# Kernel tuning notes

Measured on AMD Instinct MI355X. Metric: run time of the kernel, lower is better.

## Reference

```python
import jax, jax.numpy as jnp
import numpy as np
from jax import lax

# static dims (match init_kwargs)
B, F, C, H, W = 10, 64, 3, 180, 180   # batch=10 (hard-coded by reshape), arr_size frames
CH, OUT, NCLS = 64, 256, 5            # channel, out_size, len(ansmap)+1
K1, K2, POOL = 9, 5, 2                # second*diff, third, pool
EPS = 1e-5


def setup_inputs() -> dict:
    key = jax.random.key(0)
    ks = jax.random.split(key, 12)
    s = lambda k, shape: jax.random.normal(k, shape, dtype=jnp.float32) * 0.05
    return {
        "x": jax.random.normal(ks[0], (B, F, C, H, W), dtype=jnp.float32),
        "W1": s(ks[1], (CH, C, K1, K1)),
        "b1": s(ks[2], (CH,)),
        "W2": s(ks[3], (3, CH, K2, K2)),
        "b2": s(ks[4], (3,)),
        "gamma": jnp.ones((F,), jnp.float32),
        "beta": jnp.zeros((F,), jnp.float32),
        "Wih": s(ks[5], (3, OUT, 1)),
        "Whh": s(ks[6], (3, OUT, OUT)),
        "bih": s(ks[7], (3, OUT)),
        "bhh": s(ks[8], (3, OUT)),
        "Wl": s(ks[9], (NCLS, OUT)),
        "bl": s(ks[10], (NCLS,)),
    }


def _maxpool2(y):
    return lax.reduce_window(y, -jnp.inf, lax.max, (1, 1, POOL, POOL), (1, 1, POOL, POOL), 'VALID')


def reference(x, W1, b1, W2, b2, gamma, beta, Wih, Whh, bih, bhh, Wl, bl):
    # conv stack applied per frame; batch all B*F frames at once
    xc = x.reshape(B * F, C, H, W)
    y = lax.conv_general_dilated(xc, W1, (K1, K1), 'VALID') + b1[None, :, None, None]
    y = _maxpool2(jax.nn.relu(y))                      # [B*F, CH, 10, 10]
    y = lax.conv_general_dilated(y, W2, (K2, K2), 'VALID') + b2[None, :, None, None]
    y = _maxpool2(jax.nn.relu(y))                      # [B*F, 3, 1, 1]
    y = y.reshape(B, F, 3)

    # BatchNorm1d(arr_size) in train mode: normalize each of the F channels over (batch, length)
    mean = y.mean(axis=(0, 2), keepdims=True)
    var = y.var(axis=(0, 2), keepdims=True)
    y = (y - mean) / jnp.sqrt(var + EPS) * gamma[None, :, None] + beta[None, :, None]

    # per-sample reorder of the 3 channels by (max - min) range over time
    t = y.transpose(0, 2, 1)                           # [B, 3, F]
    rng = t.max(-1) - t.min(-1)                        # [B, 3]
    perm = jnp.argsort(rng, axis=1)                    # [B, 3]
    ts = jnp.take_along_axis(t, perm[:, :, None], axis=1)  # [B, 3, F]

    # rank r goes through RNN r; vmap the scan over the 3 RNNs
    seqs = ts.transpose(1, 2, 0)[..., None]            # [3, F, B, 1]

    def rnn_last(seq, wih, whh, bi, bh):               # seq: [F, B, 1]
        def step(h, xt):
            return jnp.tanh(xt @ wih.T + bi + h @ whh.T + bh), None
        h, _ = lax.scan(step, jnp.zeros((B, OUT), seq.dtype), seq)
        return h                                       # last hidden == output at t=-1

    lasts = jax.vmap(rnn_last)(seqs, Wih, Whh, bih, bhh)  # [3, B, OUT]
    avg = lasts.mean(axis=0)                           # AvgPool2d((3,1)) + Flatten -> [B, OUT]
    return avg @ Wl.T + bl                             # [B, NCLS]
```

## Files before the change

### kernel.cpp

```cpp
#include <hip/hip_runtime.h>

typedef __attribute__((ext_vector_type(8))) short bf16x8;
typedef __attribute__((ext_vector_type(4))) float f32x4;

#define MFMA16(a,b,c) __builtin_amdgcn_mfma_f32_16x16x32_bf16((a),(b),(c),0,0,0)

__device__ __forceinline__ unsigned short f2bf(float f){
  unsigned int u = __float_as_uint(f);
  unsigned int r = (u + 0x7fffu + ((u>>16)&1u)) >> 16;
  return (unsigned short)r;
}
__device__ __forceinline__ float bf2f(unsigned short h){
  return __uint_as_float(((unsigned int)h)<<16);
}
__device__ __forceinline__ float tanh_fast(float x){
  float e = __expf(2.f*x);
  return 1.f - 2.f/(e + 1.f);
}

#define WS_W1H   0u
#define WS_W1L   32768u
#define WS_WHHH  65536u
#define WS_WHHL  458752u
#define WS_Y1    851968u
#define WS_Y2    17235968u
#define WS_SEQ   17243648u
#define WS_LAST  17255936u

__global__ __launch_bounds__(256) void k_prep(const float* __restrict__ W1,
                                              const float* __restrict__ Whh,
                                              unsigned short* __restrict__ w1h,
                                              unsigned short* __restrict__ w1l,
                                              unsigned short* __restrict__ whh_h,
                                              unsigned short* __restrict__ whh_l){
  int t = blockIdx.x*256 + threadIdx.x;
  if (t < 2048){
    int l = t & 63, kt = (t>>6)&7, mt = t>>9;
    int co = mt*16 + (l&15);
    int k0 = kt*32 + ((l>>4)<<3);
    bf16x8 hv, lv;
    #pragma unroll
    for (int j=0;j<8;j++){
      int k = k0 + j;
      float v = (k < 243) ? W1[co*243 + k] : 0.f;
      unsigned short h = f2bf(v);
      unsigned short lo = f2bf(v - bf2f(h));
      hv[j] = (short)h; lv[j] = (short)lo;
    }
    *(bf16x8*)(w1h + (size_t)t*8) = hv;
    *(bf16x8*)(w1l + (size_t)t*8) = lv;
  } else if (t < 2048 + 24576){
    int u = t - 2048;
    int l = u & 63, kt = (u>>6)&7, nt = (u>>9)&15, rnn = u>>13;
    int o = nt*16 + (l&15);
    int k0 = kt*32 + ((l>>4)<<3);
    const float* src = Whh + ((size_t)rnn*256 + o)*256;
    bf16x8 hv, lv;
    #pragma unroll
    for (int j=0;j<8;j++){
      float v = src[k0 + j];
      unsigned short h = f2bf(v);
      unsigned short lo = f2bf(v - bf2f(h));
      hv[j] = (short)h; lv[j] = (short)lo;
    }
    *(bf16x8*)(whh_h + (size_t)u*8) = hv;
    *(bf16x8*)(whh_l + (size_t)u*8) = lv;
  }
}

__global__ __launch_bounds__(256,4) void k_conv1(const float* __restrict__ x,
                                                 const float* __restrict__ b1,
                                                 const unsigned short* __restrict__ w1h,
                                                 const unsigned short* __restrict__ w1l,
                                                 float* __restrict__ y1){
  __shared__ __align__(16) char smem[40960];
  int fr = blockIdx.x / 10, g = blockIdx.x % 10;
  int t = threadIdx.x, w = t>>6, l = t&63;

  bf16x8 ah[8], al[8];
  #pragma unroll
  for (int kt=0; kt<8; kt++){
    size_t fi = (((size_t)(w*8 + kt))*64 + l)*8;
    ah[kt] = *(const bf16x8*)(w1h + fi);
    al[kt] = *(const bf16x8*)(w1l + fi);
  }
  float bias[4];
  #pragma unroll
  for (int reg=0;reg<4;reg++) bias[reg] = b1[w*16 + ((l>>4)<<2) + reg];

  const float4* xb4 = (const float4*)x + (size_t)fr*24300 + (size_t)g*810;
  for (int i=t; i<2430; i+=256){
    int c = i/810;
    int rem = i - c*810;
    int rl = rem/45;
    int quad = rem - rl*45;
    int oyl = (rl >= 9) ? 1 : 0;
    int ky = rl - 9*oyl;
    float4 v4 = xb4[c*8100 + rem];
    int kbase = c*81 + ky*9;
    int col0 = quad<<2;
    int ox = (col0*57)>>9;
    int kx = col0 - 9*ox;
    int p = oyl*20 + ox;
    float vv[4] = {v4.x, v4.y, v4.z, v4.w};
    #pragma unroll
    for (int q=0;q<4;q++){
      int k = kbase + kx;
      int off = ((p<<9) + (k<<1)) ^ ((p&7)<<4);
      unsigned int u = __float_as_uint(vv[q]);
      *(unsigned short*)(smem + off) = (unsigned short)(u>>16);
      float lof = vv[q] - __uint_as_float(u & 0xffff0000u);
      *(unsigned short*)(smem + 20480 + off) = (unsigned short)(__float_as_uint(lof)>>16);
      kx++; if (kx==9){ kx=0; p++; }
    }
  }
  for (int i=t; i<520; i+=256){
    int p = i/13, k = 243 + (i - p*13);
    int off = ((p<<9) + (k<<1)) ^ ((p&7)<<4);
    *(unsigned short*)(smem + off) = 0;
    *(unsigned short*)(smem + 20480 + off) = 0;
  }
  __syncthreads();

  const int pbase[3] = {0, 16, 24};
  int colb = (l>>4)<<4;
  f32x4 acc[3];
  #pragma unroll
  for (int nt=0;nt<3;nt++) acc[nt] = (f32x4){0.f,0.f,0.f,0.f};
  #pragma unroll
  for (int nt=0; nt<3; nt++){
    int p = pbase[nt] + (l&15);
    int sw = (p&7)<<4;
    #pragma unroll
    for (int kt=0; kt<8; kt++){
      int off = ((p<<9) + (kt<<6) + colb) ^ sw;
      bf16x8 bh  = *(const bf16x8*)(smem + off);
      bf16x8 blo = *(const bf16x8*)(smem + 20480 + off);
      acc[nt] = MFMA16(ah[kt], bh,  acc[nt]);
      acc[nt] = MFMA16(ah[kt], blo, acc[nt]);
      acc[nt] = MFMA16(al[kt], bh,  acc[nt]);
    }
  }
  __syncthreads();

  float* poolb = (float*)smem;
  #pragma unroll
  for (int nt=0;nt<3;nt++){
    int m = l&15;
    int p = pbase[nt] + m;
    #pragma unroll
    for (int reg=0;reg<4;reg++){
      int co = w*16 + ((l>>4)<<2) + reg;
      float v = fmaxf(acc[nt][reg] + bias[reg], 0.f);
      if (nt != 2 || m >= 8) poolb[co*41 + p] = v;
    }
  }
  __syncthreads();
  for (int idx=t; idx<640; idx+=256){
    int co = idx/10, xp = idx - co*10;
    const float* pb = poolb + co*41;
    float m = fmaxf(fmaxf(pb[2*xp], pb[2*xp+1]), fmaxf(pb[20+2*xp], pb[21+2*xp]));
    y1[(size_t)fr*6400 + co*100 + g*10 + xp] = m;
  }
}

__global__ __launch_bounds__(256) void k_conv2(const float* __restrict__ y1,
                                               const float* __restrict__ W2,
                                               const float* __restrict__ b2,
                                               float* __restrict__ y2){
  __shared__ float yl[6400];
  __shared__ float w2s[4800];
  int fr = blockIdx.x, t = threadIdx.x;
  const float4* src = (const float4*)(y1 + (size_t)fr*6400);
  for (int i=t;i<1600;i+=256) ((float4*)yl)[i] = src[i];
  for (int i=t;i<1200;i+=256) ((float4*)w2s)[i] = ((const float4*)W2)[i];
  __syncthreads();
  if (t < 192){
    int o = t>>4, l16 = t&15;
    int ch = o>>2, pos = o&3;
    int oy = pos>>1, ox = pos&1;
    float s = 0.f;
    for (int i=0;i<100;i++){
      int k = l16 + (i<<4);
      int ci = k/25; int r = k - ci*25; int ky = r/5, kx = r - ky*5;
      s += yl[ci*100 + (5*oy+ky)*10 + 5*ox + kx] * w2s[ch*1600 + k];
    }
    #pragma unroll
    for (int d=1; d<16; d<<=1) s += __shfl_xor(s, d);
    float v = fmaxf(s + b2[ch], 0.f);
    v = fmaxf(v, __shfl_xor(v, 16));
    v = fmaxf(v, __shfl_xor(v, 32));
    if ((t&63)==0) y2[fr*3 + (t>>6)] = v;
  }
}

__global__ __launch_bounds__(256) void k_bn(const float* __restrict__ y2,
                                            const float* __restrict__ gamma,
                                            const float* __restrict__ beta,
                                            float* __restrict__ seq){
  __shared__ float yl[1920];
  __shared__ float af[64], bfv[64];
  __shared__ float tsb[10][3][64];
  __shared__ float rngL[10][3];
  __shared__ int   perm[10][3];
  int t = threadIdx.x;
  for (int i=t;i<1920;i+=256) yl[i] = y2[i];
  __syncthreads();
  if (t < 64){
    float mu = 0.f;
    for (int b=0;b<10;b++)
      for (int ch=0;ch<3;ch++) mu += yl[(b*64 + t)*3 + ch];
    mu *= (1.f/30.f);
    float v = 0.f;
    for (int b=0;b<10;b++)
      for (int ch=0;ch<3;ch++){ float d = yl[(b*64+t)*3+ch] - mu; v += d*d; }
    v *= (1.f/30.f);
    float rs = rsqrtf(v + 1e-5f);
    float a = gamma[t]*rs;
    af[t] = a; bfv[t] = beta[t] - mu*a;
  }
  __syncthreads();
  if (t < 30){
    int b = t/3, ch = t - b*3;
    float mx = -1e30f, mn = 1e30f;
    for (int f=0; f<64; f++){
      float v = yl[(b*64+f)*3+ch]*af[f] + bfv[f];
      tsb[b][ch][f] = v;
      mx = fmaxf(mx, v); mn = fminf(mn, v);
    }
    rngL[b][ch] = mx - mn;
  }
  __syncthreads();
  if (t < 10){
    #pragma unroll
    for (int ch=0; ch<3; ch++){
      float rc = rngL[t][ch];
      int rank = 0;
      #pragma unroll
      for (int c2=0; c2<3; c2++){
        float r2 = rngL[t][c2];
        if (r2 < rc || (r2 == rc && c2 < ch)) rank++;
      }
      perm[t][rank] = ch;
    }
  }
  __syncthreads();
  for (int idx=t; idx<3072; idx+=256){
    int r = idx>>10, rem = idx & 1023, f = rem>>4, b = rem & 15;
    float v = 0.f;
    if (b < 10) v = tsb[b][perm[b][r]][f];
    seq[idx] = v;
  }
}

__global__ __launch_bounds__(512) void k_rnn(const unsigned short* __restrict__ whh_h,
                                             const unsigned short* __restrict__ whh_l,
                                             const float* __restrict__ seq,
                                             const float* __restrict__ Wih,
                                             const float* __restrict__ bih,
                                             const float* __restrict__ bhh,
                                             float* __restrict__ lasts){
  __shared__ __align__(16) char hsm[36864];
  float* seqL = (float*)(hsm + 32768);
  int rnn = blockIdx.x;
  int t = threadIdx.x, w = t>>6, l = t&63;
  bf16x8 Bh[2][8], Bl[2][8];
  #pragma unroll
  for (int q=0;q<2;q++){
    int nt = 2*w + q;
    #pragma unroll
    for (int kt=0;kt<8;kt++){
      size_t fi = (((((size_t)rnn*16 + nt)*8) + kt)*64 + l)*8;
      Bh[q][kt] = *(const bf16x8*)(whh_h + fi);
      Bl[q][kt] = *(const bf16x8*)(whh_l + fi);
    }
  }
  int o0 = (2*w)*16 + (l&15), o1 = o0 + 16;
  float wih0 = Wih[rnn*256 + o0], wih1 = Wih[rnn*256 + o1];
  float bs0 = bih[rnn*256+o0] + bhh[rnn*256+o0];
  float bs1 = bih[rnn*256+o1] + bhh[rnn*256+o1];
  for (int i=t; i<1024; i+=512) seqL[i] = seq[rnn*1024 + i];
  float4 z4 = {0.f,0.f,0.f,0.f};
  for (int i=t; i<1024; i+=512) ((float4*)hsm)[i] = z4;
  __syncthreads();
  int arow = l&15, colb = (l>>4)<<4, sw = (arow&7)<<4;
  int b_base = (l>>4)<<2;
  for (int step=0; step<64; step++){
    char* cur = hsm + ((step&1)<<14);
    char* nxt = hsm + (((step+1)&1)<<14);
    f32x4 p0=(f32x4){0,0,0,0}, q0=p0, r0=p0, p1=p0, q1=p0, r1=p0;
    #pragma unroll
    for (int kt=0; kt<8; kt++){
      int off = ((arow<<9) + (kt<<6) + colb) ^ sw;
      bf16x8 ahv = *(const bf16x8*)(cur + off);
      bf16x8 alv = *(const bf16x8*)(cur + 8192 + off);
      p0 = MFMA16(ahv, Bh[0][kt], p0);
      q0 = MFMA16(ahv, Bl[0][kt], q0);
      r0 = MFMA16(alv, Bh[0][kt], r0);
      p1 = MFMA16(ahv, Bh[1][kt], p1);
      q1 = MFMA16(ahv, Bl[1][kt], q1);
      r1 = MFMA16(alv, Bh[1][kt], r1);
    }
    float4 sx = *(const float4*)(seqL + (step<<4) + b_base);
    float sxa[4] = {sx.x, sx.y, sx.z, sx.w};
    #pragma unroll
    for (int reg=0; reg<4; reg++){
      int b = b_base + reg;
      float a0 = (p0[reg] + q0[reg]) + r0[reg];
      float a1 = (p1[reg] + q1[reg]) + r1[reg];
      float h0 = tanh_fast(a0 + sxa[reg]*wih0 + bs0);
      float h1 = tanh_fast(a1 + sxa[reg]*wih1 + bs1);
      int wsw = (b&7)<<4;
      int off0 = ((b<<9) + (o0<<1)) ^ wsw;
      int off1 = ((b<<9) + (o1<<1)) ^ wsw;
      unsigned int u0 = __float_as_uint(h0);
      unsigned int u1 = __float_as_uint(h1);
      *(unsigned short*)(nxt + off0) = (unsigned short)(u0>>16);
      float l0 = h0 - __uint_as_float(u0 & 0xffff0000u);
      *(unsigned short*)(nxt + 8192 + off0) = (unsigned short)(__float_as_uint(l0)>>16);
      *(unsigned short*)(nxt + off1) = (unsigned short)(u1>>16);
      float l1 = h1 - __uint_as_float(u1 & 0xffff0000u);
      *(unsigned short*)(nxt + 8192 + off1) = (unsigned short)(__float_as_uint(l1)>>16);
      if (step == 63){
        lasts[((size_t)rnn*16 + b)*256 + o0] = h0;
        lasts[((size_t)rnn*16 + b)*256 + o1] = h1;
      }
    }
    __syncthreads();
  }
}

__global__ __launch_bounds__(512) void k_head(const float* __restrict__ lasts,
                                              const float* __restrict__ Wl,
                                              const float* __restrict__ bl,
                                              float* __restrict__ out){
  int t = threadIdx.x;
  if (t < 400){
    int oidx = t>>3, l8 = t&7;
    int b = oidx/5, c = oidx - b*5;
    float s = 0.f;
    for (int i=0;i<32;i++){
      int o = (l8<<5) + i;
      float avg = (lasts[(size_t)(0*16+b)*256+o] + lasts[(size_t)(1*16+b)*256+o]
                 + lasts[(size_t)(2*16+b)*256+o]) * (1.f/3.f);
      s += avg * Wl[c*256 + o];
    }
    #pragma unroll
    for (int d=1; d<8; d<<=1) s += __shfl_xor(s, d);
    if (l8 == 0) out[oidx] = s + bl[c];
  }
}

extern "C" void kernel_launch(void* const* d_in, const int* in_sizes, int n_in,
                              void* d_out, int out_size, void* d_ws, size_t ws_size,
                              hipStream_t stream){
  const float* x    = (const float*)d_in[0];
  const float* W1   = (const float*)d_in[1];
  const float* b1   = (const float*)d_in[2];
  const float* W2   = (const float*)d_in[3];
  const float* b2   = (const float*)d_in[4];
  const float* gamma= (const float*)d_in[5];
  const float* beta = (const float*)d_in[6];
  const float* Wih  = (const float*)d_in[7];
  const float* Whh  = (const float*)d_in[8];
  const float* bih  = (const float*)d_in[9];
  const float* bhh  = (const float*)d_in[10];
  const float* Wl   = (const float*)d_in[11];
  const float* bl   = (const float*)d_in[12];
  char* ws = (char*)d_ws;
  unsigned short* w1h  = (unsigned short*)(ws + WS_W1H);
  unsigned short* w1l  = (unsigned short*)(ws + WS_W1L);
  unsigned short* whhh = (unsigned short*)(ws + WS_WHHH);
  unsigned short* whhl = (unsigned short*)(ws + WS_WHHL);
  float* y1   = (float*)(ws + WS_Y1);
  float* y2   = (float*)(ws + WS_Y2);
  float* seq  = (float*)(ws + WS_SEQ);
  float* last = (float*)(ws + WS_LAST);

  hipLaunchKernelGGL(k_prep,  dim3(104),  dim3(256), 0, stream, W1, Whh, w1h, w1l, whhh, whhl);
  hipLaunchKernelGGL(k_conv1, dim3(6400), dim3(256), 0, stream, x, b1, w1h, w1l, y1);
  hipLaunchKernelGGL(k_conv2, dim3(640),  dim3(256), 0, stream, y1, W2, b2, y2);
  hipLaunchKernelGGL(k_bn,    dim3(1),    dim3(256), 0, stream, y2, gamma, beta, seq);
  hipLaunchKernelGGL(k_rnn,   dim3(3),    dim3(512), 0, stream, whhh, whhl, seq, Wih, bih, bhh, last);
  hipLaunchKernelGGL(k_head,  dim3(1),    dim3(512), 0, stream, last, Wl, bl, (float*)d_out);
}
```

Measured before the change: 193.4 us.

## Async-load conv inputs into LDS and fuse batchnorm/sort into RNN kernel

New measurement: 204.2 us. +5.6%, slower.

```diff
diff --git a/kernel.cpp b/kernel.cpp
--- a/kernel.cpp
+++ b/kernel.cpp
@@ -4,6 +4,12 @@
 typedef __attribute__((ext_vector_type(4))) float f32x4;
 
 #define MFMA16(a,b,c) __builtin_amdgcn_mfma_f32_16x16x32_bf16((a),(b),(c),0,0,0)
+
+#define AS1 __attribute__((address_space(1)))
+#define AS3 __attribute__((address_space(3)))
+__device__ __forceinline__ void async16(void* lds, const void* g){
+  __builtin_amdgcn_global_load_lds((const AS1 unsigned int*)g, (AS3 unsigned int*)lds, 16, 0, 0);
+}
 
 __device__ __forceinline__ unsigned short f2bf(float f){
   unsigned int u = __float_as_uint(f);
@@ -24,7 +30,6 @@
 #define WS_WHHL  458752u
 #define WS_Y1    851968u
 #define WS_Y2    17235968u
-#define WS_SEQ   17243648u
 #define WS_LAST  17255936u
 
 __global__ __launch_bounds__(256) void k_prep(const float* __restrict__ W1,
@@ -68,14 +73,21 @@
   }
 }
 
-__global__ __launch_bounds__(256,4) void k_conv1(const float* __restrict__ x,
+__global__ __launch_bounds__(256,2) void k_conv1(const float* __restrict__ x,
                                                  const float* __restrict__ b1,
                                                  const unsigned short* __restrict__ w1h,
                                                  const unsigned short* __restrict__ w1l,
                                                  float* __restrict__ y1){
-  __shared__ __align__(16) char smem[40960];
+  __shared__ __align__(16) char smem[79840];
   int fr = blockIdx.x / 10, g = blockIdx.x % 10;
   int t = threadIdx.x, w = t>>6, l = t&63;
+
+  const float4* xb4 = (const float4*)x + (size_t)fr*24300 + (size_t)g*810;
+  for (int i=t; i<2430; i+=256){
+    int c = i/810;
+    int rem = i - c*810;
+    async16(smem + 40960 + i*16, (const void*)(xb4 + c*8100 + rem));
+  }
 
   bf16x8 ah[8], al[8];
   #pragma unroll
@@ -88,7 +100,14 @@
   #pragma unroll
   for (int reg=0;reg<4;reg++) bias[reg] = b1[w*16 + ((l>>4)<<2) + reg];
 
-  const float4* xb4 = (const float4*)x + (size_t)fr*24300 + (size_t)g*810;
+  for (int i=t; i<520; i+=256){
+    int p = i/13, k = 243 + (i - p*13);
+    int off = ((p<<9) + (k<<1)) ^ ((p&7)<<4);
+    *(unsigned short*)(smem + off) = 0;
+    *(unsigned short*)(smem + 20480 + off) = 0;
+  }
+  __syncthreads();
+
   for (int i=t; i<2430; i+=256){
     int c = i/810;
     int rem = i - c*810;
@@ -96,7 +115,7 @@
     int quad = rem - rl*45;
     int oyl = (rl >= 9) ? 1 : 0;
     int ky = rl - 9*oyl;
-    float4 v4 = xb4[c*8100 + rem];
+    float4 v4 = *(const float4*)(smem + 40960 + i*16);
     int kbase = c*81 + ky*9;
     int col0 = quad<<2;
     int ox = (col0*57)>>9;
@@ -114,12 +133,6 @@
       kx++; if (kx==9){ kx=0; p++; }
     }
   }
-  for (int i=t; i<520; i+=256){
-    int p = i/13, k = 243 + (i - p*13);
-    int off = ((p<<9) + (k<<1)) ^ ((p&7)<<4);
-    *(unsigned short*)(smem + off) = 0;
-    *(unsigned short*)(smem + 20480 + off) = 0;
-  }
   __syncthreads();
 
   const int pbase[3] = {0, 16, 24};
@@ -168,12 +181,12 @@
                                                const float* __restrict__ W2,
                                                const float* __restrict__ b2,
                                                float* __restrict__ y2){
-  __shared__ float yl[6400];
-  __shared__ float w2s[4800];
+  __shared__ __align__(16) float yl[6400];
+  __shared__ __align__(16) float w2s[4800];
   int fr = blockIdx.x, t = threadIdx.x;
   const float4* src = (const float4*)(y1 + (size_t)fr*6400);
-  for (int i=t;i<1600;i+=256) ((float4*)yl)[i] = src[i];
-  for (int i=t;i<1200;i+=256) ((float4*)w2s)[i] = ((const float4*)W2)[i];
+  for (int i=t;i<1600;i+=256) async16(((float4*)yl) + i, (const void*)(src + i));
+  for (int i=t;i<1200;i+=256) async16(((float4*)w2s) + i, (const void*)(((const float4*)W2) + i));
   __syncthreads();
   if (t < 192){
     int o = t>>4, l16 = t&15;
@@ -194,17 +207,43 @@
   }
 }
 
-__global__ __launch_bounds__(256) void k_bn(const float* __restrict__ y2,
-                                            const float* __restrict__ gamma,
-                                            const float* __restrict__ beta,
-                                            float* __restrict__ seq){
-  __shared__ float yl[1920];
-  __shared__ float af[64], bfv[64];
-  __shared__ float tsb[10][3][64];
-  __shared__ float rngL[10][3];
-  __shared__ int   perm[10][3];
-  int t = threadIdx.x;
-  for (int i=t;i<1920;i+=256) yl[i] = y2[i];
+__global__ __launch_bounds__(512) void k_rnn(const unsigned short* __restrict__ whh_h,
+                                             const unsigned short* __restrict__ whh_l,
+                                             const float* __restrict__ y2,
+                                             const float* __restrict__ gamma,
+                                             const float* __restrict__ beta,
+                                             const float* __restrict__ Wih,
+                                             const float* __restrict__ bih,
+                                             const float* __restrict__ bhh,
+                                             float* __restrict__ lasts){
+  __shared__ __align__(16) char hsm[36864];
+  float* yl   = (float*)hsm;
+  float* af   = (float*)(hsm + 7680);
+  float* bfv  = (float*)(hsm + 7936);
+  float* rngL = (float*)(hsm + 8192);
+  int*   perm = (int*)(hsm + 8320);
+  float* tsb  = (float*)(hsm + 8448);
+  float* seqL = (float*)(hsm + 32768);
+  int rnn = blockIdx.x;
+  int t = threadIdx.x, w = t>>6, l = t&63;
+
+  bf16x8 Bh[2][8], Bl[2][8];
+  #pragma unroll
+  for (int q=0;q<2;q++){
+    int nt = 2*w + q;
+    #pragma unroll
+    for (int kt=0;kt<8;kt++){
+      size_t fi = (((((size_t)rnn*16 + nt)*8) + kt)*64 + l)*8;
+      Bh[q][kt] = *(const bf16x8*)(whh_h + fi);
+      Bl[q][kt] = *(const bf16x8*)(whh_l + fi);
+    }
+  }
+  int o0 = (2*w)*16 + (l&15), o1 = o0 + 16;
+  float wih0 = Wih[rnn*256 + o0], wih1 = Wih[rnn*256 + o1];
+  float bs0 = bih[rnn*256+o0] + bhh[rnn*256+o0];
+  float bs1 = bih[rnn*256+o1] + bhh[rnn*256+o1];
+
+  for (int i=t;i<1920;i+=512) yl[i] = y2[i];
   __syncthreads();
   if (t < 64){
     float mu = 0.f;
@@ -225,61 +264,34 @@
     float mx = -1e30f, mn = 1e30f;
     for (int f=0; f<64; f++){
       float v = yl[(b*64+f)*3+ch]*af[f] + bfv[f];
-      tsb[b][ch][f] = v;
+      tsb[(b*3+ch)*64 + f] = v;
       mx = fmaxf(mx, v); mn = fminf(mn, v);
     }
-    rngL[b][ch] = mx - mn;
+    rngL[b*3+ch] = mx - mn;
   }
   __syncthreads();
   if (t < 10){
     #pragma unroll
     for (int ch=0; ch<3; ch++){
-      float rc = rngL[t][ch];
+      float rc = rngL[t*3+ch];
       int rank = 0;
       #pragma unroll
       for (int c2=0; c2<3; c2++){
-        float r2 = rngL[t][c2];
+        float r2 = rngL[t*3+c2];
         if (r2 < rc || (r2 == rc && c2 < ch)) rank++;
       }
-      perm[t][rank] = ch;
-    }
-  }
-  __syncthreads();
-  for (int idx=t; idx<3072; idx+=256){
-    int r = idx>>10, rem = idx & 1023, f = rem>>4, b = rem & 15;
+      perm[t*3+rank] = ch;
+    }
+  }
+  __syncthreads();
+  for (int i=t;i<1024;i+=512){
+    int step = i>>4, b = i&15;
     float v = 0.f;
-    if (b < 10) v = tsb[b][perm[b][r]][f];
-    seq[idx] = v;
-  }
-}
-
-__global__ __launch_bounds__(512) void k_rnn(const unsigned short* __restrict__ whh_h,
-                                             const unsigned short* __restrict__ whh_l,
-                                             const float* __restrict__ seq,
-                                             const float* __restrict__ Wih,
-                                             const float* __restrict__ bih,
-                                             const float* __restrict__ bhh,
-                                             float* __restrict__ lasts){
-  __shared__ __align__(16) char hsm[36864];
-  float* seqL = (float*)(hsm + 32768);
-  int rnn = blockIdx.x;
-  int t = threadIdx.x, w = t>>6, l = t&63;
-  bf16x8 Bh[2][8], Bl[2][8];
-  #pragma unroll
-  for (int q=0;q<2;q++){
-    int nt = 2*w + q;
-    #pragma unroll
-    for (int kt=0;kt<8;kt++){
-      size_t fi = (((((size_t)rnn*16 + nt)*8) + kt)*64 + l)*8;
-      Bh[q][kt] = *(const bf16x8*)(whh_h + fi);
-      Bl[q][kt] = *(const bf16x8*)(whh_l + fi);
-    }
-  }
-  int o0 = (2*w)*16 + (l&15), o1 = o0 + 16;
-  float wih0 = Wih[rnn*256 + o0], wih1 = Wih[rnn*256 + o1];
-  float bs0 = bih[rnn*256+o0] + bhh[rnn*256+o0];
-  float bs1 = bih[rnn*256+o1] + bhh[rnn*256+o1];
-  for (int i=t; i<1024; i+=512) seqL[i] = seq[rnn*1024 + i];
+    if (b < 10){ int p = perm[b*3 + rnn]; v = tsb[(b*3+p)*64 + step]; }
+    seqL[i] = v;
+  }
+  __syncthreads();
+
   float4 z4 = {0.f,0.f,0.f,0.f};
   for (int i=t; i<1024; i+=512) ((float4*)hsm)[i] = z4;
   __syncthreads();
@@ -374,13 +386,11 @@
   unsigned short* whhl = (unsigned short*)(ws + WS_WHHL);
   float* y1   = (float*)(ws + WS_Y1);
   float* y2   = (float*)(ws + WS_Y2);
-  float* seq  = (float*)(ws + WS_SEQ);
   float* last = (float*)(ws + WS_LAST);
 
   hipLaunchKernelGGL(k_prep,  dim3(104),  dim3(256), 0, stream, W1, Whh, w1h, w1l, whhh, whhl);
   hipLaunchKernelGGL(k_conv1, dim3(6400), dim3(256), 0, stream, x, b1, w1h, w1l, y1);
   hipLaunchKernelGGL(k_conv2, dim3(640),  dim3(256), 0, stream, y1, W2, b2, y2);
-  hipLaunchKernelGGL(k_bn,    dim3(1),    dim3(256), 0, stream, y2, gamma, beta, seq);
-  hipLaunchKernelGGL(k_rnn,   dim3(3),    dim3(512), 0, stream, whhh, whhl, seq, Wih, bih, bhh, last);
+  hipLaunchKernelGGL(k_rnn,   dim3(3),    dim3(512), 0, stream, whhh, whhl, y2, gamma, beta, Wih, bih, bhh, last);
   hipLaunchKernelGGL(k_head,  dim3(1),    dim3(512), 0, stream, last, Wl, bl, (float*)d_out);
 }
```
